# Performance work log

Hardware: AMD Instinct MI355X
Metric: run time of the kernel (lower is better)

## Reference

```python
import jax, jax.numpy as jnp
import numpy as np

N_HEAD = 16
N_EMBD = 1024
LOCAL_WINDOW = 256
GLOBAL_IDX = np.array([0, 1, 2, 3], dtype=np.int64)


def build_mask(T):
    # [T, T] boolean: local causal window + global rows/cols (Longformer-style)
    i = np.arange(T)[:, None]
    j = np.arange(T)[None, :]
    causal = j <= i
    local = causal & (j >= i - LOCAL_WINDOW + 1)
    g_row = np.isin(np.arange(T), GLOBAL_IDX)[:, None]  # global queries attend to all past
    g_col = np.isin(np.arange(T), GLOBAL_IDX)[None, :]  # global keys attended by all later
    mask = local | (g_row & causal) | (g_col & causal)
    return jnp.asarray(mask)


def setup_inputs() -> dict:
    key = jax.random.key(0)
    k1, k2, k3 = jax.random.split(key, 3)
    B, T, C = 2, 2048, N_EMBD
    x = jax.random.normal(k1, (B, T, C), dtype=jnp.float32)
    w_attn = jax.random.normal(k2, (3 * C, C), dtype=jnp.float32) * (1.0 / np.sqrt(C))
    w_proj = jax.random.normal(k3, (C, C), dtype=jnp.float32) * (1.0 / np.sqrt(C))
    return {"x": x, "w_attn": w_attn, "w_proj": w_proj}


def reference(x, w_attn, w_proj):
    B, T, C = x.shape
    H, D = N_HEAD, C // N_HEAD
    qkv = jnp.einsum('btc,fc->btf', x, w_attn)  # [B,T,3C], torch Linear: x @ W.T
    q, k, v = jnp.split(qkv, 3, axis=-1)
    # [B,H,T,D]
    q = q.reshape(B, T, H, D).transpose(0, 2, 1, 3)
    k = k.reshape(B, T, H, D).transpose(0, 2, 1, 3)
    v = v.reshape(B, T, H, D).transpose(0, 2, 1, 3)
    mask = build_mask(T)  # [T,T] bool, constant
    scale = 1.0 / np.sqrt(D)
    att = jnp.einsum('bhqd,bhkd->bhqk', q, k) * scale
    att = jnp.where(mask, att, jnp.finfo(att.dtype).min)
    att = jax.nn.softmax(att, axis=-1)
    y = jnp.einsum('bhqk,bhkd->bhqd', att, v)
    y = y.transpose(0, 2, 1, 3).reshape(B, T, C)
    return jnp.einsum('btc,oc->bto', y, w_proj)
```

## Files before the change

### kernel.cpp

```cpp
#include <hip/hip_runtime.h>


#define NHD   16
#define CEMB  1024
#define C3    3072
#define DH    64
#define WIN   256
#define NGLB  4
#define TB    256

typedef __attribute__((ext_vector_type(8))) short  short8v;
typedef __attribute__((ext_vector_type(4))) float  f32x4;
typedef __attribute__((ext_vector_type(8))) unsigned short ushort8v;

__device__ __forceinline__ unsigned short f2bf_rn(float f) {
    unsigned int u = __float_as_uint(f);
    u += 0x7fffu + ((u >> 16) & 1u);
    return (unsigned short)(u >> 16);
}
__device__ __forceinline__ float bf2f(unsigned short h) {
    return __uint_as_float(((unsigned int)h) << 16);
}

__global__ __launch_bounds__(TB)
void split_bf16_kernel(const float* __restrict__ in, unsigned short* __restrict__ hi,
                       unsigned short* __restrict__ lo, int n8) {
    for (int i = blockIdx.x * blockDim.x + threadIdx.x; i < n8;
         i += gridDim.x * blockDim.x) {
        float4 v0 = ((const float4*)in)[2 * i];
        float4 v1 = ((const float4*)in)[2 * i + 1];
        float f[8] = {v0.x, v0.y, v0.z, v0.w, v1.x, v1.y, v1.z, v1.w};
        ushort8v h, l;
#pragma unroll
        for (int j = 0; j < 8; ++j) {
            unsigned short hb = f2bf_rn(f[j]);
            h[j] = hb;
            l[j] = f2bf_rn(f[j] - bf2f(hb));
        }
        *(ushort8v*)&hi[(size_t)i * 8] = h;
        *(ushort8v*)&lo[(size_t)i * 8] = l;
    }
}

__device__ __forceinline__ void g2l16(const void* g, void* l) {
    __builtin_amdgcn_global_load_lds(
        (const __attribute__((address_space(1))) void*)g,
        (__attribute__((address_space(3))) void*)l, 16, 0, 0);
}

template<int OUTMODE>
__global__ __launch_bounds__(TB)
void gemm_split_mfma_kernel(const unsigned short* __restrict__ Ah,
                            const unsigned short* __restrict__ Al,
                            const unsigned short* __restrict__ Bh,
                            const unsigned short* __restrict__ Bl,
                            float* __restrict__ Cf,
                            unsigned short* __restrict__ Ch,
                            unsigned short* __restrict__ Cl,
                            int M, int N, int K) {
    __shared__ unsigned short lds[4][128 * 32];

    const int tid  = threadIdx.x;
    const int wave = tid >> 6;
    const int lane = tid & 63;
    const int nbn  = N >> 7;
    const int mb   = blockIdx.x / nbn;
    const int nb   = blockIdx.x % nbn;

    const int row0 = (wave)     * 16 + (lane >> 2);
    const int row1 = (wave + 4) * 16 + (lane >> 2);
    const int koff = (lane & 3) * 8;
    const size_t aoff0 = (size_t)(mb * 128 + row0) * K + koff;
    const size_t aoff1 = (size_t)(mb * 128 + row1) * K + koff;
    const size_t boff0 = (size_t)(nb * 128 + row0) * K + koff;
    const size_t boff1 = (size_t)(nb * 128 + row1) * K + koff;
    const int l0 = wave * 512;
    const int l1 = (wave + 4) * 512;

    const int wr = wave >> 1, wc = wave & 1;
    const int fr = lane & 15;
    const int ks = (lane >> 4) * 8;

    f32x4 acc[4][4];
#pragma unroll
    for (int m = 0; m < 4; ++m)
#pragma unroll
        for (int n = 0; n < 4; ++n) acc[m][n] = (f32x4){0.f, 0.f, 0.f, 0.f};

    for (int kt = 0; kt < K; kt += 32) {
        __syncthreads();
        g2l16(Ah + aoff0 + kt, &lds[0][l0]);
        g2l16(Ah + aoff1 + kt, &lds[0][l1]);
        g2l16(Al + aoff0 + kt, &lds[1][l0]);
        g2l16(Al + aoff1 + kt, &lds[1][l1]);
        g2l16(Bh + boff0 + kt, &lds[2][l0]);
        g2l16(Bh + boff1 + kt, &lds[2][l1]);
        g2l16(Bl + boff0 + kt, &lds[3][l0]);
        g2l16(Bl + boff1 + kt, &lds[3][l1]);
        __syncthreads();

        short8v ah[4], al[4], bh[4], bl[4];
#pragma unroll
        for (int m = 0; m < 4; ++m) {
            const int r = (wr * 64 + m * 16 + fr) * 32 + ks;
            ah[m] = *(const short8v*)&lds[0][r];
            al[m] = *(const short8v*)&lds[1][r];
        }
#pragma unroll
        for (int n = 0; n < 4; ++n) {
            const int r = (wc * 64 + n * 16 + fr) * 32 + ks;
            bh[n] = *(const short8v*)&lds[2][r];
            bl[n] = *(const short8v*)&lds[3][r];
        }
#pragma unroll
        for (int m = 0; m < 4; ++m)
#pragma unroll
            for (int n = 0; n < 4; ++n) {
                acc[m][n] = __builtin_amdgcn_mfma_f32_16x16x32_bf16(
                    ah[m], bh[n], acc[m][n], 0, 0, 0);
                acc[m][n] = __builtin_amdgcn_mfma_f32_16x16x32_bf16(
                    ah[m], bl[n], acc[m][n], 0, 0, 0);
                acc[m][n] = __builtin_amdgcn_mfma_f32_16x16x32_bf16(
                    al[m], bh[n], acc[m][n], 0, 0, 0);
            }
    }

    const int cr = (lane >> 4) * 4;
#pragma unroll
    for (int m = 0; m < 4; ++m)
#pragma unroll
        for (int n = 0; n < 4; ++n) {
#pragma unroll
            for (int r = 0; r < 4; ++r) {
                const int row = mb * 128 + wr * 64 + m * 16 + cr + r;
                const int col = nb * 128 + wc * 64 + n * 16 + fr;
                if constexpr (OUTMODE == 0) {
                    Cf[(size_t)row * N + col] = acc[m][n][r];
                } else {
                    float v = acc[m][n][r];
                    if (col < CEMB) v *= 0.125f;
                    unsigned short hb = f2bf_rn(v);
                    Ch[(size_t)row * N + col] = hb;
                    Cl[(size_t)row * N + col] = f2bf_rn(v - bf2f(hb));
                }
            }
        }
}

__global__ __launch_bounds__(TB)
void attn_mfma_kernel(const unsigned short* __restrict__ qkvh,
                      const unsigned short* __restrict__ qkvl,
                      unsigned short* __restrict__ yh,
                      unsigned short* __restrict__ yl, int T) {
    __shared__ unsigned short Kh[4096], Kl[4096], VTh[4096], VTl[4096],
                              Ph[4096], Pl[4096];

    const int tid = threadIdx.x;
    const int wv  = tid >> 6, ln = tid & 63;
    const int g   = ln >> 4, fr = ln & 15;
    const int nq  = T >> 6;
    const int qt  = blockIdx.x % nq;
    const int bh  = blockIdx.x / nq;
    const int h   = bh % NHD, b = bh / NHD;
    const int qs  = qt << 6;
    const size_t bT = (size_t)b * T;

    const size_t qbase = (bT + qs + wv * 16 + fr) * C3 + h * DH;
    short8v qfh[2], qfl[2];
    qfh[0] = *(const short8v*)(qkvh + qbase + g * 8);
    qfh[1] = *(const short8v*)(qkvh + qbase + 32 + g * 8);
    qfl[0] = *(const short8v*)(qkvl + qbase + g * 8);
    qfl[1] = *(const short8v*)(qkvl + qbase + 32 + g * 8);

    float mrow[4], lrow[4];
    f32x4 acc_o[4];
#pragma unroll
    for (int r = 0; r < 4; ++r) { mrow[r] = -3.0e38f; lrow[r] = 0.f; }
#pragma unroll
    for (int j = 0; j < 4; ++j) acc_o[j] = (f32x4){0.f, 0.f, 0.f, 0.f};

    int kt_first = 0;
    const int wstart = qs - (WIN - 1);
    if (wstart > 0) kt_first = wstart >> 6;
    const int has_g = (kt_first > 0) ? 1 : 0;
    const int npass = qt - kt_first + 1 + has_g;

    const int srow = tid >> 2;
    const int sc   = tid & 3;
    const int kidx0 = srow * 64 + ((sc * 8)       ^ ((srow & 7) << 3));
    const int kidx1 = srow * 64 + (((sc + 4) * 8) ^ ((srow & 7) << 3));

    short8v kh0, kh1, kl0, kl1, vh0, vh1, vl0, vl1;
    auto load_tile = [&](int k0) {
        const size_t kb = (bT + k0 + srow) * C3 + CEMB + h * DH;
        kh0 = *(const short8v*)(qkvh + kb + sc * 8);
        kh1 = *(const short8v*)(qkvh + kb + (sc + 4) * 8);
        kl0 = *(const short8v*)(qkvl + kb + sc * 8);
        kl1 = *(const short8v*)(qkvl + kb + (sc + 4) * 8);
        const size_t vb = (bT + k0 + srow) * C3 + 2 * CEMB + h * DH + sc * 16;
        vh0 = *(const short8v*)(qkvh + vb);
        vh1 = *(const short8v*)(qkvh + vb + 8);
        vl0 = *(const short8v*)(qkvl + vb);
        vl1 = *(const short8v*)(qkvl + vb + 8);
    };
    auto kt_of = [&](int p) { return (has_g && p == 0) ? 0 : (kt_first + p - has_g); };

    load_tile(kt_of(0) * 64);

    for (int pass = 0; pass < npass; ++pass) {
        const int k0 = kt_of(pass) * 64;

        __syncthreads();
        *(short8v*)&Kh[kidx0] = kh0; *(short8v*)&Kh[kidx1] = kh1;
        *(short8v*)&Kl[kidx0] = kl0; *(short8v*)&Kl[kidx1] = kl1;
#pragma unroll
        for (int e = 0; e < 8; ++e) {
            const int d1 = sc * 16 + e, d2 = sc * 16 + 8 + e;
            const int i1 = d1 * 64 + (srow ^ (((d1 ^ (d1 >> 3)) & 7) << 3));
            const int i2 = d2 * 64 + (srow ^ (((d2 ^ (d2 >> 3)) & 7) << 3));
            VTh[i1] = (unsigned short)vh0[e]; VTh[i2] = (unsigned short)vh1[e];
            VTl[i1] = (unsigned short)vl0[e]; VTl[i2] = (unsigned short)vl1[e];
        }
        __syncthreads();

        if (pass + 1 < npass) load_tile(kt_of(pass + 1) * 64);

        f32x4 sa[4];
#pragma unroll
        for (int j = 0; j < 4; ++j) sa[j] = (f32x4){0.f, 0.f, 0.f, 0.f};
#pragma unroll
        for (int kk = 0; kk < 2; ++kk) {
#pragma unroll
            for (int j = 0; j < 4; ++j) {
                const int krow = j * 16 + fr;
                const int off  = (kk * 32 + g * 8) ^ ((krow & 7) << 3);
                short8v bhf = *(const short8v*)&Kh[krow * 64 + off];
                short8v blf = *(const short8v*)&Kl[krow * 64 + off];
                sa[j] = __builtin_amdgcn_mfma_f32_16x16x32_bf16(qfh[kk], bhf, sa[j], 0, 0, 0);
                sa[j] = __builtin_amdgcn_mfma_f32_16x16x32_bf16(qfh[kk], blf, sa[j], 0, 0, 0);
                sa[j] = __builtin_amdgcn_mfma_f32_16x16x32_bf16(qfl[kk], bhf, sa[j], 0, 0, 0);
            }
        }

#pragma unroll
        for (int r = 0; r < 4; ++r) {
            const int qloc = wv * 16 + g * 4 + r;
            const int qi   = qs + qloc;
            const int wlo  = qi - (WIN - 1);
            float mx = mrow[r];
            float s[4];
#pragma unroll
            for (int j = 0; j < 4; ++j) {
                const int kj = k0 + j * 16 + fr;
                const bool valid = (kj <= qi) && ((kj >= wlo) || (kj < NGLB));
                s[j] = valid ? sa[j][r] : -3.0e38f;
                mx = fmaxf(mx, s[j]);
            }
#pragma unroll
            for (int off = 1; off < 16; off <<= 1)
                mx = fmaxf(mx, __shfl_xor(mx, off, 64));
            const float alpha = __expf(mrow[r] - mx);
            float rsum = 0.f;
            unsigned short phv[4], plv[4];
#pragma unroll
            for (int j = 0; j < 4; ++j) {
                const float p = (s[j] > -1.0e38f) ? __expf(s[j] - mx) : 0.f;
                rsum += p;
                const unsigned short hb = f2bf_rn(p);
                phv[j] = hb; plv[j] = f2bf_rn(p - bf2f(hb));
            }
#pragma unroll
            for (int off = 1; off < 16; off <<= 1)
                rsum += __shfl_xor(rsum, off, 64);
            lrow[r] = lrow[r] * alpha + rsum;
            mrow[r] = mx;
#pragma unroll
            for (int j = 0; j < 4; ++j) {
                acc_o[j][r] *= alpha;
                const int key = j * 16 + fr;
                const int idx = qloc * 64 + (key ^ ((qloc & 7) << 3));
                Ph[idx] = phv[j]; Pl[idx] = plv[j];
            }
        }

#pragma unroll
        for (int kk = 0; kk < 2; ++kk) {
            const int qloc = wv * 16 + fr;
            const int poff = (kk * 32 + g * 8) ^ ((qloc & 7) << 3);
            short8v pah = *(const short8v*)&Ph[qloc * 64 + poff];
            short8v pal = *(const short8v*)&Pl[qloc * 64 + poff];
#pragma unroll
            for (int j = 0; j < 4; ++j) {
                const int d   = j * 16 + fr;
                const int voff = (kk * 32 + g * 8) ^ (((d ^ (d >> 3)) & 7) << 3);
                short8v vfh = *(const short8v*)&VTh[d * 64 + voff];
                short8v vfl = *(const short8v*)&VTl[d * 64 + voff];
                acc_o[j] = __builtin_amdgcn_mfma_f32_16x16x32_bf16(pah, vfh, acc_o[j], 0, 0, 0);
                acc_o[j] = __builtin_amdgcn_mfma_f32_16x16x32_bf16(pah, vfl, acc_o[j], 0, 0, 0);
                acc_o[j] = __builtin_amdgcn_mfma_f32_16x16x32_bf16(pal, vfh, acc_o[j], 0, 0, 0);
            }
        }
    }

    float inv[4];
#pragma unroll
    for (int r = 0; r < 4; ++r) inv[r] = 1.0f / lrow[r];
#pragma unroll
    for (int j = 0; j < 4; ++j)
#pragma unroll
        for (int r = 0; r < 4; ++r) {
            const float o = acc_o[j][r] * inv[r];
            const size_t yi = (bT + qs + wv * 16 + g * 4 + r) * (size_t)CEMB
                            + h * DH + j * 16 + fr;
            const unsigned short hb = f2bf_rn(o);
            yh[yi] = hb; yl[yi] = f2bf_rn(o - bf2f(hb));
        }
}

extern "C" void kernel_launch(void* const* d_in, const int* in_sizes, int n_in,
                              void* d_out, int out_size, void* d_ws, size_t ws_size,
                              hipStream_t stream) {
    const float* x      = (const float*)d_in[0];
    const float* w_attn = (const float*)d_in[1];
    const float* w_proj = (const float*)d_in[2];
    float* out = (float*)d_out;

    const int T = 2048;
    const int B = in_sizes[0] / (T * CEMB);
    const int M = B * T;

    unsigned short* qkvh = (unsigned short*)d_ws;
    unsigned short* qkvl = qkvh + (size_t)M * C3;
    unsigned short* yh   = qkvl + (size_t)M * C3;
    unsigned short* yl   = yh   + (size_t)M * CEMB;
    unsigned short* xh   = yl   + (size_t)M * CEMB;
    unsigned short* xl   = xh   + (size_t)M * CEMB;
    unsigned short* wah  = xl   + (size_t)M * CEMB;
    unsigned short* wal  = wah  + (size_t)C3 * CEMB;
    unsigned short* wph  = wal  + (size_t)C3 * CEMB;
    unsigned short* wpl  = wph  + (size_t)CEMB * CEMB;

    split_bf16_kernel<<<2048, TB, 0, stream>>>(x, xh, xl, M * CEMB / 8);
    split_bf16_kernel<<<1536, TB, 0, stream>>>(w_attn, wah, wal, C3 * CEMB / 8);
    split_bf16_kernel<<<512,  TB, 0, stream>>>(w_proj, wph, wpl, CEMB * CEMB / 8);

    gemm_split_mfma_kernel<1><<<dim3((M / 128) * (C3 / 128)), dim3(TB), 0, stream>>>(
        xh, xl, wah, wal, nullptr, qkvh, qkvl, M, C3, CEMB);

    attn_mfma_kernel<<<dim3(B * NHD * (T / 64)), dim3(TB), 0, stream>>>(
        qkvh, qkvl, yh, yl, T);

    gemm_split_mfma_kernel<0><<<dim3((M / 128) * (CEMB / 128)), dim3(TB), 0, stream>>>(
        yh, yl, wph, wpl, out, nullptr, nullptr, M, CEMB, CEMB);
}
```

Baseline: 278.6 us.

## Double-buffer GEMM LDS tiles, swizzle LDS layout, fuse split kernels

The split-bf16 GEMM now double-buffers its LDS tiles, issuing the global-to-LDS loads for the next K step before computing the current one, so each iteration needs one barrier instead of two. It also XOR-swizzles the 16-byte chunk offsets in LDS, applied the same way on write and read, to reduce bank conflicts on the fragment reads. The three hi/lo split launches are merged into one kernel to cut launch overhead. LDS use per block doubles, which may lower occupancy.

```diff
diff --git a/kernel.cpp b/kernel.cpp
--- a/kernel.cpp
+++ b/kernel.cpp
@@ -23,22 +23,31 @@
 }
 
 __global__ __launch_bounds__(TB)
-void split_bf16_kernel(const float* __restrict__ in, unsigned short* __restrict__ hi,
-                       unsigned short* __restrict__ lo, int n8) {
-    for (int i = blockIdx.x * blockDim.x + threadIdx.x; i < n8;
+void split3_kernel(const float* __restrict__ x, const float* __restrict__ wa,
+                   const float* __restrict__ wp,
+                   unsigned short* __restrict__ xh, unsigned short* __restrict__ xl,
+                   unsigned short* __restrict__ wah, unsigned short* __restrict__ wal,
+                   unsigned short* __restrict__ wph, unsigned short* __restrict__ wpl,
+                   int n8x, int n8a, int n8p) {
+    const int total = n8x + n8a + n8p;
+    for (int i = blockIdx.x * blockDim.x + threadIdx.x; i < total;
          i += gridDim.x * blockDim.x) {
-        float4 v0 = ((const float4*)in)[2 * i];
-        float4 v1 = ((const float4*)in)[2 * i + 1];
+        const float* src; unsigned short *ph, *pl; int j;
+        if (i < n8x)            { src = x;  ph = xh;  pl = xl;  j = i; }
+        else if (i < n8x + n8a) { src = wa; ph = wah; pl = wal; j = i - n8x; }
+        else                    { src = wp; ph = wph; pl = wpl; j = i - n8x - n8a; }
+        float4 v0 = ((const float4*)src)[2 * j];
+        float4 v1 = ((const float4*)src)[2 * j + 1];
         float f[8] = {v0.x, v0.y, v0.z, v0.w, v1.x, v1.y, v1.z, v1.w};
         ushort8v h, l;
 #pragma unroll
-        for (int j = 0; j < 8; ++j) {
-            unsigned short hb = f2bf_rn(f[j]);
-            h[j] = hb;
-            l[j] = f2bf_rn(f[j] - bf2f(hb));
-        }
-        *(ushort8v*)&hi[(size_t)i * 8] = h;
-        *(ushort8v*)&lo[(size_t)i * 8] = l;
+        for (int e = 0; e < 8; ++e) {
+            unsigned short hb = f2bf_rn(f[e]);
+            h[e] = hb;
+            l[e] = f2bf_rn(f[e] - bf2f(hb));
+        }
+        *(ushort8v*)&ph[(size_t)j * 8] = h;
+        *(ushort8v*)&pl[(size_t)j * 8] = l;
     }
 }
 
@@ -58,7 +67,7 @@
                             unsigned short* __restrict__ Ch,
                             unsigned short* __restrict__ Cl,
                             int M, int N, int K) {
-    __shared__ unsigned short lds[4][128 * 32];
+    __shared__ unsigned short lds[2][4][128 * 32];
 
     const int tid  = threadIdx.x;
     const int wave = tid >> 6;
@@ -69,7 +78,7 @@
 
     const int row0 = (wave)     * 16 + (lane >> 2);
     const int row1 = (wave + 4) * 16 + (lane >> 2);
-    const int koff = (lane & 3) * 8;
+    const int koff = (((lane & 3) ^ ((lane >> 3) & 3)) << 3);
     const size_t aoff0 = (size_t)(mb * 128 + row0) * K + koff;
     const size_t aoff1 = (size_t)(mb * 128 + row1) * K + koff;
     const size_t boff0 = (size_t)(nb * 128 + row0) * K + koff;
@@ -79,7 +88,8 @@
 
     const int wr = wave >> 1, wc = wave & 1;
     const int fr = lane & 15;
-    const int ks = (lane >> 4) * 8;
+    const int g  = lane >> 4;
+    const int ksel = (fr >> 1) & 3;
 
     f32x4 acc[4][4];
 #pragma unroll
@@ -87,30 +97,37 @@
 #pragma unroll
         for (int n = 0; n < 4; ++n) acc[m][n] = (f32x4){0.f, 0.f, 0.f, 0.f};
 
+    auto STAGE = [&](int bi, int kt) {
+        g2l16(Ah + aoff0 + kt, &lds[bi][0][l0]);
+        g2l16(Ah + aoff1 + kt, &lds[bi][0][l1]);
+        g2l16(Al + aoff0 + kt, &lds[bi][1][l0]);
+        g2l16(Al + aoff1 + kt, &lds[bi][1][l1]);
+        g2l16(Bh + boff0 + kt, &lds[bi][2][l0]);
+        g2l16(Bh + boff1 + kt, &lds[bi][2][l1]);
+        g2l16(Bl + boff0 + kt, &lds[bi][3][l0]);
+        g2l16(Bl + boff1 + kt, &lds[bi][3][l1]);
+    };
+
+    STAGE(0, 0);
+    __syncthreads();
+    int cur = 0;
+
     for (int kt = 0; kt < K; kt += 32) {
-        __syncthreads();
-        g2l16(Ah + aoff0 + kt, &lds[0][l0]);
-        g2l16(Ah + aoff1 + kt, &lds[0][l1]);
-        g2l16(Al + aoff0 + kt, &lds[1][l0]);
-        g2l16(Al + aoff1 + kt, &lds[1][l1]);
-        g2l16(Bh + boff0 + kt, &lds[2][l0]);
-        g2l16(Bh + boff1 + kt, &lds[2][l1]);
-        g2l16(Bl + boff0 + kt, &lds[3][l0]);
-        g2l16(Bl + boff1 + kt, &lds[3][l1]);
-        __syncthreads();
-
+        if (kt + 32 < K) STAGE(cur ^ 1, kt + 32);
+
+        const int co = ((g ^ ksel) << 3);
         short8v ah[4], al[4], bh[4], bl[4];
 #pragma unroll
         for (int m = 0; m < 4; ++m) {
-            const int r = (wr * 64 + m * 16 + fr) * 32 + ks;
-            ah[m] = *(const short8v*)&lds[0][r];
-            al[m] = *(const short8v*)&lds[1][r];
+            const int r = (wr * 64 + m * 16 + fr) * 32 + co;
+            ah[m] = *(const short8v*)&lds[cur][0][r];
+            al[m] = *(const short8v*)&lds[cur][1][r];
         }
 #pragma unroll
         for (int n = 0; n < 4; ++n) {
-            const int r = (wc * 64 + n * 16 + fr) * 32 + ks;
-            bh[n] = *(const short8v*)&lds[2][r];
-            bl[n] = *(const short8v*)&lds[3][r];
+            const int r = (wc * 64 + n * 16 + fr) * 32 + co;
+            bh[n] = *(const short8v*)&lds[cur][2][r];
+            bl[n] = *(const short8v*)&lds[cur][3][r];
         }
 #pragma unroll
         for (int m = 0; m < 4; ++m)
@@ -123,6 +140,9 @@
                 acc[m][n] = __builtin_amdgcn_mfma_f32_16x16x32_bf16(
                     al[m], bh[n], acc[m][n], 0, 0, 0);
             }
+
+        __syncthreads();
+        cur ^= 1;
     }
 
     const int cr = (lane >> 4) * 4;
@@ -340,9 +360,12 @@
     unsigned short* wph  = wal  + (size_t)C3 * CEMB;
     unsigned short* wpl  = wph  + (size_t)CEMB * CEMB;
 
-    split_bf16_kernel<<<2048, TB, 0, stream>>>(x, xh, xl, M * CEMB / 8);
-    split_bf16_kernel<<<1536, TB, 0, stream>>>(w_attn, wah, wal, C3 * CEMB / 8);
-    split_bf16_kernel<<<512,  TB, 0, stream>>>(w_proj, wph, wpl, CEMB * CEMB / 8);
+    const int n8x = M * CEMB / 8;
+    const int n8a = C3 * CEMB / 8;
+    const int n8p = CEMB * CEMB / 8;
+    split3_kernel<<<2048, TB, 0, stream>>>(x, w_attn, w_proj,
+                                           xh, xl, wah, wal, wph, wpl,
+                                           n8x, n8a, n8p);
 
     gemm_split_mfma_kernel<1><<<dim3((M / 128) * (C3 / 128)), dim3(TB), 0, stream>>>(
         xh, xl, wah, wal, nullptr, qkvh, qkvl, M, C3, CEMB);
```

Result: faster. 247.3 us (-11.2%).
